# Performance work log

Measured on AMD Instinct MI355X. Metric: run time of the kernel, lower is better.

Reference implementation:

```python
import jax, jax.numpy as jnp
import numpy as np

NEG = -1e20

def _rope(x):
    # x: (N, L, H, D). Original buffers use inv_freq over D with D/2 entries;
    # sin/cos tiled to full D to broadcast (original code's einsum was under-specified for 4D).
    L, D = x.shape[1], x.shape[3]
    inv_freq = 1.0 / (10000.0 ** (jnp.arange(0, D, 2, dtype=jnp.float32) / D))
    t = jnp.arange(L, dtype=jnp.float32)
    freqs = t[:, None] * inv_freq[None, :]            # (L, D/2)
    sin = jnp.concatenate([jnp.sin(freqs)] * 2, -1)[None, :, None, :]  # (1,L,1,D)
    cos = jnp.concatenate([jnp.cos(freqs)] * 2, -1)[None, :, None, :]
    return x * cos + jnp.flip(x, -1) * sin

def setup_inputs() -> dict:
    key = jax.random.key(0)
    ks = jax.random.split(key, 8)
    N, L, E, H = 2, 1024, 2048, 16
    D = E // H
    s = 0.02
    return {
        "values": jax.random.normal(ks[0], (N, L, E), jnp.float32),
        "keys": jax.random.normal(ks[1], (N, L, E), jnp.float32),
        "queries": jax.random.normal(ks[2], (N, L, E), jnp.float32),
        "mask": jax.random.randint(ks[3], (N, 1, L, L), 0, 2, jnp.int32),
        "Wv": jax.random.normal(ks[4], (D, D), jnp.float32) * s,
        "Wk": jax.random.normal(ks[5], (D, D), jnp.float32) * s,
        "Wq": jax.random.normal(ks[6], (D, D), jnp.float32) * s,
        "Wo": jax.random.normal(ks[7], (E, E), jnp.float32) * s,
        "bo": jnp.zeros((E,), jnp.float32),
    }

def reference(values, keys, queries, mask, Wv, Wk, Wq, Wo, bo):
    N, L, E = queries.shape
    H = 16
    D = E // H
    v = values.reshape(N, L, H, D)
    k = keys.reshape(N, L, H, D)
    q = queries.reshape(N, L, H, D)
    q = _rope(q)
    k = _rope(k)
    # per-head linears (nn.Linear: x @ W.T)
    v = jnp.einsum('nlhd,od->nlho', v, Wv)
    k = jnp.einsum('nlhd,od->nlho', k, Wk)
    q = jnp.einsum('nlhd,od->nlho', q, Wq)
    energy = jnp.einsum('nqhd,nkhd->nhqk', q, k)
    energy = jnp.where(mask == 0, NEG, energy)
    attn = jax.nn.softmax(energy / jnp.sqrt(jnp.float32(E)), axis=3)
    out = jnp.einsum('nhqk,nkhd->nqhd', attn, v).reshape(N, L, E)
    return out @ Wo.T + bo
```

## Files before the change

### kernel.cpp

```cpp
#include <hip/hip_runtime.h>

#define LQ 1024
#define EMB 2048
#define NH 16
#define HD 128
#define RSCALE 0.022097086912079608f

typedef unsigned short u16x8 __attribute__((ext_vector_type(8)));
typedef __bf16 bf16x8 __attribute__((ext_vector_type(8)));
typedef float f32x4 __attribute__((ext_vector_type(4)));

__device__ __forceinline__ unsigned short f2b(float f){
  unsigned int x = __float_as_uint(f);
  return (unsigned short)((x + 0x7fffu + ((x >> 16) & 1u)) >> 16);
}
__device__ __forceinline__ bf16x8 as_bf(u16x8 u){
  union { u16x8 u; bf16x8 b; } c; c.u = u; return c.b;
}

__global__ __launch_bounds__(256) void k_sincos(float* __restrict__ cosT,
                                                float* __restrict__ sinT){
  int idx = blockIdx.x * 256 + threadIdx.x;
  int l = idx >> 7, d = idx & 127, j = d & 63;
  float inv = 1.0f / powf(10000.0f, (float)(2 * j) * 0.0078125f);
  float ang = (float)l * inv;
  cosT[idx] = cosf(ang);
  sinT[idx] = sinf(ang);
}

__global__ __launch_bounds__(256) void k_cvt(const float* __restrict__ src,
                                             unsigned short* __restrict__ dst){
  int i = (blockIdx.x * 256 + threadIdx.x) * 4;
  float4 f = *(const float4*)&src[i];
  ushort4 u;
  u.x = f2b(f.x); u.y = f2b(f.y); u.z = f2b(f.z); u.w = f2b(f.w);
  *(ushort4*)&dst[i] = u;
}

__global__ __launch_bounds__(256) void k_maskpack(const int* __restrict__ M,
                                                  unsigned long long* __restrict__ Mb){
  int w_idx = blockIdx.x * 4 + (threadIdx.x >> 6);
  int lane = threadIdx.x & 63;
  int n = w_idx >> 14, row = (w_idx >> 4) & 1023, wc = w_idx & 15;
  int v = M[(size_t)n * (LQ * LQ) + (size_t)row * LQ + wc * 64 + lane];
  unsigned long long b = __ballot(v != 0);
  if (lane == 0) Mb[w_idx] = b;
}

__global__ __launch_bounds__(256) void k_proj(
    const float* __restrict__ vals, const float* __restrict__ keys,
    const float* __restrict__ qrys,
    const float* __restrict__ Wv, const float* __restrict__ Wk,
    const float* __restrict__ Wq,
    const float* __restrict__ cosT, const float* __restrict__ sinT,
    unsigned short* __restrict__ vp, unsigned short* __restrict__ kp,
    unsigned short* __restrict__ qp)
{
  __shared__ unsigned short Xs[64 * 136];
  __shared__ unsigned short Ws[128 * 136];
  int t = threadIdx.x;
  int which = blockIdx.y;
  const float* X; const float* W; unsigned short* OUT; bool rope;
  if (which == 0)      { X = vals; W = Wv; OUT = vp; rope = false; }
  else if (which == 1) { X = keys; W = Wk; OUT = kp; rope = true;  }
  else                 { X = qrys; W = Wq; OUT = qp; rope = true;  }
  int m0 = blockIdx.x * 64;

  #pragma unroll
  for (int i = 0; i < 8; ++i) {
    int ci = t + 256 * i;
    int row = ci >> 4, ch = ci & 15;
    float4 a = *(const float4*)&W[row * 128 + ch * 8];
    float4 b = *(const float4*)&W[row * 128 + ch * 8 + 4];
    u16x8 u;
    u[0]=f2b(a.x); u[1]=f2b(a.y); u[2]=f2b(a.z); u[3]=f2b(a.w);
    u[4]=f2b(b.x); u[5]=f2b(b.y); u[6]=f2b(b.z); u[7]=f2b(b.w);
    *(u16x8*)&Ws[row * 136 + ch * 8] = u;
  }
  #pragma unroll
  for (int i = 0; i < 8; ++i) {
    int fi = t + 256 * i;
    int row = fi >> 5, dq = (fi & 31) * 4;
    int gr = m0 + row;
    float4 x = *(const float4*)&X[(size_t)gr * HD + dq];
    ushort4 u;
    if (rope) {
      int l = (gr >> 4) & 1023;
      float4 xm = *(const float4*)&X[(size_t)gr * HD + (124 - dq)];
      float4 c  = *(const float4*)&cosT[l * HD + dq];
      float4 s  = *(const float4*)&sinT[l * HD + dq];
      u.x = f2b(x.x * c.x + xm.w * s.x);
      u.y = f2b(x.y * c.y + xm.z * s.y);
      u.z = f2b(x.z * c.z + xm.y * s.z);
      u.w = f2b(x.w * c.w + xm.x * s.w);
    } else {
      u.x = f2b(x.x); u.y = f2b(x.y); u.z = f2b(x.z); u.w = f2b(x.w);
    }
    *(ushort4*)&Xs[row * 136 + dq] = u;
  }
  __syncthreads();

  int w = t >> 6, lane = t & 63, quad = lane >> 4, n16 = lane & 15;
  f32x4 of[4][2];
  #pragma unroll
  for (int a = 0; a < 4; ++a)
    { of[a][0] = (f32x4){0.f,0.f,0.f,0.f}; of[a][1] = (f32x4){0.f,0.f,0.f,0.f}; }

  #pragma unroll
  for (int kd = 0; kd < 4; ++kd) {
    bf16x8 bfr[2];
    #pragma unroll
    for (int b2 = 0; b2 < 2; ++b2)
      bfr[b2] = as_bf(*(const u16x8*)&Ws[(w * 32 + b2 * 16 + n16) * 136 + kd * 32 + quad * 8]);
    #pragma unroll
    for (int a = 0; a < 4; ++a) {
      bf16x8 af = as_bf(*(const u16x8*)&Xs[(a * 16 + n16) * 136 + kd * 32 + quad * 8]);
      of[a][0] = __builtin_amdgcn_mfma_f32_16x16x32_bf16(af, bfr[0], of[a][0], 0, 0, 0);
      of[a][1] = __builtin_amdgcn_mfma_f32_16x16x32_bf16(af, bfr[1], of[a][1], 0, 0, 0);
    }
  }

  #pragma unroll
  for (int a = 0; a < 4; ++a) {
    #pragma unroll
    for (int b2 = 0; b2 < 2; ++b2) {
      #pragma unroll
      for (int r = 0; r < 4; ++r) {
        int m = m0 + a * 16 + quad * 4 + r;
        int n = m >> 14, l = (m >> 4) & 1023, h = m & 15;
        int o = w * 32 + b2 * 16 + n16;
        OUT[(((size_t)(n * NH + h)) * LQ + l) * HD + o] = f2b(of[a][b2][r]);
      }
    }
  }
}

__global__ __launch_bounds__(256) void k_vtrans(const unsigned short* __restrict__ vp,
                                                unsigned short* __restrict__ vt){
  __shared__ unsigned short Ls[64 * 136];
  int t = threadIdx.x;
  int l0 = blockIdx.x * 64;
  size_t base = (size_t)blockIdx.y * LQ * HD;
  #pragma unroll
  for (int i = 0; i < 4; ++i) {
    int ci = t + 256 * i;
    int row = ci >> 4, ch = ci & 15;
    *(u16x8*)&Ls[row * 136 + ch * 8] =
        *(const u16x8*)&vp[base + (size_t)(l0 + row) * HD + ch * 8];
  }
  __syncthreads();
  #pragma unroll
  for (int i = 0; i < 4; ++i) {
    int idx = t + 256 * i;
    int d = idx & 127, lc = idx >> 7;
    u16x8 pk;
    #pragma unroll
    for (int j = 0; j < 8; ++j) pk[j] = Ls[(lc * 8 + j) * 136 + d];
    *(u16x8*)&vt[base + (size_t)d * LQ + l0 + lc * 8] = pk;
  }
}

__global__ __launch_bounds__(256) void k_attn(
    const unsigned short* __restrict__ qp, const unsigned short* __restrict__ kp,
    const unsigned short* __restrict__ vt, const unsigned long long* __restrict__ Mb,
    unsigned short* __restrict__ ao)
{
  __shared__ unsigned short Ks[64 * 136];
  __shared__ unsigned short Vt[128 * 72];
  __shared__ unsigned short Ss[4 * 16 * 72];
  int t = threadIdx.x, w = t >> 6, lane = t & 63, quad = lane >> 4, n16 = lane & 15;
  int bh = blockIdx.y, nIdx = bh >> 4, h = bh & 15;
  int q0 = blockIdx.x * 64;
  size_t base = (size_t)bh * LQ * HD;
  const unsigned short* Q = qp + base;
  const unsigned short* K = kp + base;
  const unsigned short* V = vt + base;

  bf16x8 qf[4];
  #pragma unroll
  for (int kd = 0; kd < 4; ++kd)
    qf[kd] = as_bf(*(const u16x8*)&Q[(size_t)(q0 + w * 16 + n16) * HD + kd * 32 + quad * 8]);

  const unsigned long long* MbRow =
      Mb + ((size_t)nIdx * LQ + q0 + w * 16 + quad * 4) * 16;

  f32x4 of[8];
  #pragma unroll
  for (int c = 0; c < 8; ++c) of[c] = (f32x4){0.f, 0.f, 0.f, 0.f};
  float lp[4] = {0.f, 0.f, 0.f, 0.f};
  unsigned short* Ssw = Ss + w * 1152;

  u16x8 pk[4], pv[4];
  #pragma unroll
  for (int i = 0; i < 4; ++i) {
    int ci = t + 256 * i;
    pk[i] = *(const u16x8*)&K[(size_t)(ci >> 4) * HD + (ci & 15) * 8];
    pv[i] = *(const u16x8*)&V[(size_t)(ci >> 3) * LQ + (ci & 7) * 8];
  }

  for (int kt = 0; kt < 16; ++kt) {
    __syncthreads();
    #pragma unroll
    for (int i = 0; i < 4; ++i) {
      int ci = t + 256 * i;
      *(u16x8*)&Ks[(ci >> 4) * 136 + (ci & 15) * 8] = pk[i];
      *(u16x8*)&Vt[(ci >> 3) * 72 + (ci & 7) * 8]  = pv[i];
    }
    __syncthreads();
    if (kt < 15) {
      int k1 = (kt + 1) * 64;
      #pragma unroll
      for (int i = 0; i < 4; ++i) {
        int ci = t + 256 * i;
        pk[i] = *(const u16x8*)&K[(size_t)(k1 + (ci >> 4)) * HD + (ci & 15) * 8];
        pv[i] = *(const u16x8*)&V[(size_t)(ci >> 3) * LQ + k1 + (ci & 7) * 8];
      }
    }
    unsigned long long mw[4];
    #pragma unroll
    for (int r = 0; r < 4; ++r) mw[r] = MbRow[r * 16 + kt];

    f32x4 sf[4];
    #pragma unroll
    for (int c = 0; c < 4; ++c) sf[c] = (f32x4){0.f, 0.f, 0.f, 0.f};
    #pragma unroll
    for (int kd = 0; kd < 4; ++kd) {
      #pragma unroll
      for (int c = 0; c < 4; ++c) {
        bf16x8 kv = as_bf(*(const u16x8*)&Ks[(c * 16 + n16) * 136 + kd * 32 + quad * 8]);
        sf[c] = __builtin_amdgcn_mfma_f32_16x16x32_bf16(qf[kd], kv, sf[c], 0, 0, 0);
      }
    }
    #pragma unroll
    for (int r = 0; r < 4; ++r) {
      #pragma unroll
      for (int c = 0; c < 4; ++c) {
        int bit = (int)((mw[r] >> (c * 16 + n16)) & 1ull);
        float p = bit ? __expf(sf[c][r] * RSCALE) : 0.f;
        lp[r] += p;
        Ssw[(quad * 4 + r) * 72 + c * 16 + n16] = f2b(p);
      }
    }
    #pragma unroll
    for (int ks = 0; ks < 2; ++ks) {
      bf16x8 pa = as_bf(*(const u16x8*)&Ssw[n16 * 72 + ks * 32 + quad * 8]);
      #pragma unroll
      for (int c2 = 0; c2 < 8; ++c2) {
        bf16x8 vv = as_bf(*(const u16x8*)&Vt[(c2 * 16 + n16) * 72 + ks * 32 + quad * 8]);
        of[c2] = __builtin_amdgcn_mfma_f32_16x16x32_bf16(pa, vv, of[c2], 0, 0, 0);
      }
    }
  }

  #pragma unroll
  for (int r = 0; r < 4; ++r) {
    float s = lp[r];
    #pragma unroll
    for (int off = 1; off < 16; off <<= 1) s += __shfl_xor(s, off, 16);
    lp[r] = 1.0f / fmaxf(s, 1e-30f);
  }
  #pragma unroll
  for (int c2 = 0; c2 < 8; ++c2) {
    #pragma unroll
    for (int r = 0; r < 4; ++r) {
      ao[((size_t)(nIdx * LQ + q0 + w * 16 + quad * 4 + r)) * EMB + h * HD + c2 * 16 + n16] =
          f2b(of[c2][r] * lp[r]);
    }
  }
}

__global__ __launch_bounds__(256) void k_outproj(
    const unsigned short* __restrict__ ao, const unsigned short* __restrict__ Wob,
    const float* __restrict__ bo, float* __restrict__ out)
{
  __shared__ unsigned short As[64 * 40];
  __shared__ unsigned short Bs[128 * 40];
  int t = threadIdx.x;
  int w = t >> 6, lane = t & 63, quad = lane >> 4, n16 = lane & 15;
  int m0 = blockIdx.x * 64, o0 = blockIdx.y * 128;

  f32x4 of[4][2];
  #pragma unroll
  for (int a = 0; a < 4; ++a)
    { of[a][0] = (f32x4){0.f,0.f,0.f,0.f}; of[a][1] = (f32x4){0.f,0.f,0.f,0.f}; }

  for (int k0 = 0; k0 < EMB; k0 += 32) {
    __syncthreads();
    {
      int row = t >> 2, ch = t & 3;
      *(u16x8*)&As[row * 40 + ch * 8] =
          *(const u16x8*)&ao[(size_t)(m0 + row) * EMB + k0 + ch * 8];
    }
    #pragma unroll
    for (int i = 0; i < 2; ++i) {
      int li = t + 256 * i;
      int row = li >> 2, ch = li & 3;
      *(u16x8*)&Bs[row * 40 + ch * 8] =
          *(const u16x8*)&Wob[(size_t)(o0 + row) * EMB + k0 + ch * 8];
    }
    __syncthreads();
    bf16x8 af[4], bfr[2];
    #pragma unroll
    for (int a = 0; a < 4; ++a)
      af[a] = as_bf(*(const u16x8*)&As[(a * 16 + n16) * 40 + quad * 8]);
    #pragma unroll
    for (int b = 0; b < 2; ++b)
      bfr[b] = as_bf(*(const u16x8*)&Bs[(w * 32 + b * 16 + n16) * 40 + quad * 8]);
    #pragma unroll
    for (int a = 0; a < 4; ++a) {
      #pragma unroll
      for (int b = 0; b < 2; ++b)
        of[a][b] = __builtin_amdgcn_mfma_f32_16x16x32_bf16(af[a], bfr[b], of[a][b], 0, 0, 0);
    }
  }

  float bb[2] = { bo[o0 + w * 32 + n16], bo[o0 + w * 32 + 16 + n16] };
  #pragma unroll
  for (int a = 0; a < 4; ++a) {
    #pragma unroll
    for (int b = 0; b < 2; ++b) {
      #pragma unroll
      for (int r = 0; r < 4; ++r) {
        out[(size_t)(m0 + a * 16 + quad * 4 + r) * EMB + o0 + w * 32 + b * 16 + n16] =
            of[a][b][r] + bb[b];
      }
    }
  }
}

extern "C" void kernel_launch(void* const* d_in, const int* in_sizes, int n_in,
                              void* d_out, int out_size, void* d_ws, size_t ws_size,
                              hipStream_t stream) {
  (void)in_sizes; (void)n_in; (void)out_size; (void)ws_size;
  const float* vals = (const float*)d_in[0];
  const float* keys = (const float*)d_in[1];
  const float* qrys = (const float*)d_in[2];
  const int*   mask = (const int*)d_in[3];
  const float* Wv   = (const float*)d_in[4];
  const float* Wk   = (const float*)d_in[5];
  const float* Wq   = (const float*)d_in[6];
  const float* Wo   = (const float*)d_in[7];
  const float* bo   = (const float*)d_in[8];
  float* out = (float*)d_out;

  unsigned short* U  = (unsigned short*)d_ws;
  unsigned short* qp = U;
  unsigned short* kp = U + 4194304;
  unsigned short* vp = U + 8388608;
  unsigned short* vt = U + 12582912;
  unsigned short* ao = U + 16777216;
  unsigned short* Wob= U + 20971520;
  unsigned long long* Mb = (unsigned long long*)(U + 25165824);
  float* cosT = (float*)(U + 25296896);
  float* sinT = cosT + 131072;

  k_sincos  <<<dim3(512),    dim3(256), 0, stream>>>(cosT, sinT);
  k_cvt     <<<dim3(4096),   dim3(256), 0, stream>>>(Wo, Wob);
  k_maskpack<<<dim3(8192),   dim3(256), 0, stream>>>(mask, Mb);
  k_proj    <<<dim3(512, 3), dim3(256), 0, stream>>>(vals, keys, qrys, Wv, Wk, Wq,
                                                     cosT, sinT, vp, kp, qp);
  k_vtrans  <<<dim3(16, 32), dim3(256), 0, stream>>>(vp, vt);
  k_attn    <<<dim3(16, 32), dim3(256), 0, stream>>>(qp, kp, vt, Mb, ao);
  k_outproj <<<dim3(32, 16), dim3(256), 0, stream>>>(ao, Wob, bo, out);
}
```

Before: 223.5 us.

## Use direct global-to-LDS loads with XOR swizzle, fuse prep kernels, retile outproj

Merges the Wo conversion and mask packing into one launch, and drops the sincos kernel by computing rope tables in shared memory inside the projection kernel. Attention and output projection now stage K/V and GEMM tiles with global_load_lds and XOR-swizzled unpadded LDS layouts. The output projection moves to a 128x128 tile with a 64-wide K step. This cuts launch count, register-staged copies and LDS bank conflicts. In exchange, the attention loop loses its register prefetch of the next tile, so loads are no longer overlapped with compute, and sin/cos is recomputed in every block.

Measured after the change: 225.6 us. About the same (+1.0%).

```diff
diff --git a/kernel.cpp b/kernel.cpp
--- a/kernel.cpp
+++ b/kernel.cpp
@@ -10,6 +10,12 @@
 typedef __bf16 bf16x8 __attribute__((ext_vector_type(8)));
 typedef float f32x4 __attribute__((ext_vector_type(4)));
 
+typedef const __attribute__((address_space(1))) unsigned int* gas_t;
+typedef __attribute__((address_space(3))) unsigned int* las_t;
+
+__device__ __forceinline__ void glds16(const void* g, void* l){
+  __builtin_amdgcn_global_load_lds((gas_t)g, (las_t)l, 16, 0, 0);
+}
 __device__ __forceinline__ unsigned short f2b(float f){
   unsigned int x = __float_as_uint(f);
   return (unsigned short)((x + 0x7fffu + ((x >> 16) & 1u)) >> 16);
@@ -18,33 +24,25 @@
   union { u16x8 u; bf16x8 b; } c; c.u = u; return c.b;
 }
 
-__global__ __launch_bounds__(256) void k_sincos(float* __restrict__ cosT,
-                                                float* __restrict__ sinT){
-  int idx = blockIdx.x * 256 + threadIdx.x;
-  int l = idx >> 7, d = idx & 127, j = d & 63;
-  float inv = 1.0f / powf(10000.0f, (float)(2 * j) * 0.0078125f);
-  float ang = (float)l * inv;
-  cosT[idx] = cosf(ang);
-  sinT[idx] = sinf(ang);
-}
-
-__global__ __launch_bounds__(256) void k_cvt(const float* __restrict__ src,
-                                             unsigned short* __restrict__ dst){
-  int i = (blockIdx.x * 256 + threadIdx.x) * 4;
-  float4 f = *(const float4*)&src[i];
-  ushort4 u;
-  u.x = f2b(f.x); u.y = f2b(f.y); u.z = f2b(f.z); u.w = f2b(f.w);
-  *(ushort4*)&dst[i] = u;
-}
-
-__global__ __launch_bounds__(256) void k_maskpack(const int* __restrict__ M,
-                                                  unsigned long long* __restrict__ Mb){
-  int w_idx = blockIdx.x * 4 + (threadIdx.x >> 6);
-  int lane = threadIdx.x & 63;
-  int n = w_idx >> 14, row = (w_idx >> 4) & 1023, wc = w_idx & 15;
-  int v = M[(size_t)n * (LQ * LQ) + (size_t)row * LQ + wc * 64 + lane];
-  unsigned long long b = __ballot(v != 0);
-  if (lane == 0) Mb[w_idx] = b;
+__global__ __launch_bounds__(256) void k_prep(const float* __restrict__ Wo,
+                                              unsigned short* __restrict__ Wob,
+                                              const int* __restrict__ M,
+                                              unsigned long long* __restrict__ Mb){
+  int bx = blockIdx.x, t = threadIdx.x;
+  if (bx < 4096) {
+    int i = (bx * 256 + t) * 4;
+    float4 f = *(const float4*)&Wo[i];
+    ushort4 u;
+    u.x = f2b(f.x); u.y = f2b(f.y); u.z = f2b(f.z); u.w = f2b(f.w);
+    *(ushort4*)&Wob[i] = u;
+  } else {
+    int w_idx = (bx - 4096) * 4 + (t >> 6);
+    int lane = t & 63;
+    int n = w_idx >> 14, row = (w_idx >> 4) & 1023, wc = w_idx & 15;
+    int v = M[(size_t)n * (LQ * LQ) + (size_t)row * LQ + wc * 64 + lane];
+    unsigned long long b = __ballot(v != 0);
+    if (lane == 0) Mb[w_idx] = b;
+  }
 }
 
 __global__ __launch_bounds__(256) void k_proj(
@@ -52,12 +50,12 @@
     const float* __restrict__ qrys,
     const float* __restrict__ Wv, const float* __restrict__ Wk,
     const float* __restrict__ Wq,
-    const float* __restrict__ cosT, const float* __restrict__ sinT,
     unsigned short* __restrict__ vp, unsigned short* __restrict__ kp,
     unsigned short* __restrict__ qp)
 {
   __shared__ unsigned short Xs[64 * 136];
   __shared__ unsigned short Ws[128 * 136];
+  __shared__ float scC[4 * 128], scS[4 * 128];
   int t = threadIdx.x;
   int which = blockIdx.y;
   const float* X; const float* W; unsigned short* OUT; bool rope;
@@ -77,6 +75,19 @@
     u[4]=f2b(b.x); u[5]=f2b(b.y); u[6]=f2b(b.z); u[7]=f2b(b.w);
     *(u16x8*)&Ws[row * 136 + ch * 8] = u;
   }
+  if (rope) {
+    int l0 = (blockIdx.x * 4) & 1023;
+    #pragma unroll
+    for (int i = 0; i < 2; ++i) {
+      int idx = t + 256 * i;
+      int li = idx >> 7, d = idx & 127, j = d & 63;
+      float inv = 1.0f / powf(10000.0f, (float)(2 * j) * 0.0078125f);
+      float ang = (float)(l0 + li) * inv;
+      scC[idx] = cosf(ang);
+      scS[idx] = sinf(ang);
+    }
+  }
+  __syncthreads();
   #pragma unroll
   for (int i = 0; i < 8; ++i) {
     int fi = t + 256 * i;
@@ -85,10 +96,10 @@
     float4 x = *(const float4*)&X[(size_t)gr * HD + dq];
     ushort4 u;
     if (rope) {
-      int l = (gr >> 4) & 1023;
+      int li = row >> 4;
       float4 xm = *(const float4*)&X[(size_t)gr * HD + (124 - dq)];
-      float4 c  = *(const float4*)&cosT[l * HD + dq];
-      float4 s  = *(const float4*)&sinT[l * HD + dq];
+      float4 c  = *(const float4*)&scC[li * 128 + dq];
+      float4 s  = *(const float4*)&scS[li * 128 + dq];
       u.x = f2b(x.x * c.x + xm.w * s.x);
       u.y = f2b(x.y * c.y + xm.z * s.y);
       u.z = f2b(x.z * c.z + xm.y * s.z);
@@ -165,8 +176,8 @@
     const unsigned short* __restrict__ vt, const unsigned long long* __restrict__ Mb,
     unsigned short* __restrict__ ao)
 {
-  __shared__ unsigned short Ks[64 * 136];
-  __shared__ unsigned short Vt[128 * 72];
+  __shared__ unsigned short Ks[64 * 128];
+  __shared__ unsigned short Vt[128 * 64];
   __shared__ unsigned short Ss[4 * 16 * 72];
   int t = threadIdx.x, w = t >> 6, lane = t & 63, quad = lane >> 4, n16 = lane & 15;
   int bh = blockIdx.y, nIdx = bh >> 4, h = bh & 15;
@@ -189,36 +200,23 @@
   for (int c = 0; c < 8; ++c) of[c] = (f32x4){0.f, 0.f, 0.f, 0.f};
   float lp[4] = {0.f, 0.f, 0.f, 0.f};
   unsigned short* Ssw = Ss + w * 1152;
-
-  u16x8 pk[4], pv[4];
-  #pragma unroll
-  for (int i = 0; i < 4; ++i) {
-    int ci = t + 256 * i;
-    pk[i] = *(const u16x8*)&K[(size_t)(ci >> 4) * HD + (ci & 15) * 8];
-    pv[i] = *(const u16x8*)&V[(size_t)(ci >> 3) * LQ + (ci & 7) * 8];
-  }
+  int ub = (t & 192);
 
   for (int kt = 0; kt < 16; ++kt) {
+    int k0 = kt * 64;
     __syncthreads();
     #pragma unroll
     for (int i = 0; i < 4; ++i) {
       int ci = t + 256 * i;
-      *(u16x8*)&Ks[(ci >> 4) * 136 + (ci & 15) * 8] = pk[i];
-      *(u16x8*)&Vt[(ci >> 3) * 72 + (ci & 7) * 8]  = pv[i];
-    }
+      int krow = ci >> 4, kslot = ci & 15, kch = kslot ^ (krow & 7);
+      glds16(&K[(size_t)(k0 + krow) * HD + kch * 8], &Ks[(ub + 256 * i) * 8]);
+      int vrow = ci >> 3, vslot = ci & 7, vch = vslot ^ (vrow & 7);
+      glds16(&V[(size_t)vrow * LQ + k0 + vch * 8], &Vt[(ub + 256 * i) * 8]);
+    }
+    unsigned long long mw[4];
+    #pragma unroll
+    for (int r = 0; r < 4; ++r) mw[r] = MbRow[r * 16 + kt];
     __syncthreads();
-    if (kt < 15) {
-      int k1 = (kt + 1) * 64;
-      #pragma unroll
-      for (int i = 0; i < 4; ++i) {
-        int ci = t + 256 * i;
-        pk[i] = *(const u16x8*)&K[(size_t)(k1 + (ci >> 4)) * HD + (ci & 15) * 8];
-        pv[i] = *(const u16x8*)&V[(size_t)(ci >> 3) * LQ + k1 + (ci & 7) * 8];
-      }
-    }
-    unsigned long long mw[4];
-    #pragma unroll
-    for (int r = 0; r < 4; ++r) mw[r] = MbRow[r * 16 + kt];
 
     f32x4 sf[4];
     #pragma unroll
@@ -227,7 +225,8 @@
     for (int kd = 0; kd < 4; ++kd) {
       #pragma unroll
       for (int c = 0; c < 4; ++c) {
-        bf16x8 kv = as_bf(*(const u16x8*)&Ks[(c * 16 + n16) * 136 + kd * 32 + quad * 8]);
+        int slot = (kd * 4 + quad) ^ (n16 & 7);
+        bf16x8 kv = as_bf(*(const u16x8*)&Ks[(c * 16 + n16) * 128 + slot * 8]);
         sf[c] = __builtin_amdgcn_mfma_f32_16x16x32_bf16(qf[kd], kv, sf[c], 0, 0, 0);
       }
     }
@@ -246,7 +245,8 @@
       bf16x8 pa = as_bf(*(const u16x8*)&Ssw[n16 * 72 + ks * 32 + quad * 8]);
       #pragma unroll
       for (int c2 = 0; c2 < 8; ++c2) {
-        bf16x8 vv = as_bf(*(const u16x8*)&Vt[(c2 * 16 + n16) * 72 + ks * 32 + quad * 8]);
+        int slot = (ks * 4 + quad) ^ (n16 & 7);
+        bf16x8 vv = as_bf(*(const u16x8*)&Vt[(c2 * 16 + n16) * 64 + slot * 8]);
         of[c2] = __builtin_amdgcn_mfma_f32_16x16x32_bf16(pa, vv, of[c2], 0, 0, 0);
       }
     }
@@ -273,56 +273,64 @@
     const unsigned short* __restrict__ ao, const unsigned short* __restrict__ Wob,
     const float* __restrict__ bo, float* __restrict__ out)
 {
-  __shared__ unsigned short As[64 * 40];
-  __shared__ unsigned short Bs[128 * 40];
+  __shared__ unsigned short As[128 * 64];
+  __shared__ unsigned short Bs[128 * 64];
   int t = threadIdx.x;
   int w = t >> 6, lane = t & 63, quad = lane >> 4, n16 = lane & 15;
-  int m0 = blockIdx.x * 64, o0 = blockIdx.y * 128;
-
-  f32x4 of[4][2];
+  int wm = w >> 1, wo = w & 1;
+  int m0 = blockIdx.x * 128, o0 = blockIdx.y * 128;
+  int ub = (t & 192);
+
+  f32x4 of[4][4];
   #pragma unroll
   for (int a = 0; a < 4; ++a)
-    { of[a][0] = (f32x4){0.f,0.f,0.f,0.f}; of[a][1] = (f32x4){0.f,0.f,0.f,0.f}; }
-
-  for (int k0 = 0; k0 < EMB; k0 += 32) {
+    #pragma unroll
+    for (int b = 0; b < 4; ++b) of[a][b] = (f32x4){0.f, 0.f, 0.f, 0.f};
+
+  for (int k0 = 0; k0 < EMB; k0 += 64) {
     __syncthreads();
-    {
-      int row = t >> 2, ch = t & 3;
-      *(u16x8*)&As[row * 40 + ch * 8] =
-          *(const u16x8*)&ao[(size_t)(m0 + row) * EMB + k0 + ch * 8];
-    }
-    #pragma unroll
-    for (int i = 0; i < 2; ++i) {
-      int li = t + 256 * i;
-      int row = li >> 2, ch = li & 3;
-      *(u16x8*)&Bs[row * 40 + ch * 8] =
-          *(const u16x8*)&Wob[(size_t)(o0 + row) * EMB + k0 + ch * 8];
+    #pragma unroll
+    for (int i = 0; i < 4; ++i) {
+      int ci = t + 256 * i;
+      int row = ci >> 3, slot = ci & 7, ch = slot ^ (row & 7);
+      glds16(&ao [(size_t)(m0 + row) * EMB + k0 + ch * 8], &As[(ub + 256 * i) * 8]);
+      glds16(&Wob[(size_t)(o0 + row) * EMB + k0 + ch * 8], &Bs[(ub + 256 * i) * 8]);
     }
     __syncthreads();
-    bf16x8 af[4], bfr[2];
-    #pragma unroll
-    for (int a = 0; a < 4; ++a)
-      af[a] = as_bf(*(const u16x8*)&As[(a * 16 + n16) * 40 + quad * 8]);
-    #pragma unroll
-    for (int b = 0; b < 2; ++b)
-      bfr[b] = as_bf(*(const u16x8*)&Bs[(w * 32 + b * 16 + n16) * 40 + quad * 8]);
-    #pragma unroll
-    for (int a = 0; a < 4; ++a) {
-      #pragma unroll
-      for (int b = 0; b < 2; ++b)
-        of[a][b] = __builtin_amdgcn_mfma_f32_16x16x32_bf16(af[a], bfr[b], of[a][b], 0, 0, 0);
-    }
-  }
-
-  float bb[2] = { bo[o0 + w * 32 + n16], bo[o0 + w * 32 + 16 + n16] };
+    #pragma unroll
+    for (int kd = 0; kd < 2; ++kd) {
+      bf16x8 af[4], bf[4];
+      #pragma unroll
+      for (int a = 0; a < 4; ++a) {
+        int row = wm * 64 + a * 16 + n16;
+        int slot = (kd * 4 + quad) ^ (n16 & 7);
+        af[a] = as_bf(*(const u16x8*)&As[row * 64 + slot * 8]);
+      }
+      #pragma unroll
+      for (int b = 0; b < 4; ++b) {
+        int row = wo * 64 + b * 16 + n16;
+        int slot = (kd * 4 + quad) ^ (n16 & 7);
+        bf[b] = as_bf(*(const u16x8*)&Bs[row * 64 + slot * 8]);
+      }
+      #pragma unroll
+      for (int a = 0; a < 4; ++a)
+        #pragma unroll
+        for (int b = 0; b < 4; ++b)
+          of[a][b] = __builtin_amdgcn_mfma_f32_16x16x32_bf16(af[a], bf[b], of[a][b], 0, 0, 0);
+    }
+  }
+
+  float bb[4];
+  #pragma unroll
+  for (int b = 0; b < 4; ++b) bb[b] = bo[o0 + wo * 64 + b * 16 + n16];
   #pragma unroll
   for (int a = 0; a < 4; ++a) {
     #pragma unroll
-    for (int b = 0; b < 2; ++b) {
+    for (int b = 0; b < 4; ++b) {
       #pragma unroll
       for (int r = 0; r < 4; ++r) {
-        out[(size_t)(m0 + a * 16 + quad * 4 + r) * EMB + o0 + w * 32 + b * 16 + n16] =
-            of[a][b][r] + bb[b];
+        out[(size_t)(m0 + wm * 64 + a * 16 + quad * 4 + r) * EMB
+            + o0 + wo * 64 + b * 16 + n16] = of[a][b][r] + bb[b];
       }
     }
   }
@@ -351,15 +359,11 @@
   unsigned short* ao = U + 16777216;
   unsigned short* Wob= U + 20971520;
   unsigned long long* Mb = (unsigned long long*)(U + 25165824);
-  float* cosT = (float*)(U + 25296896);
-  float* sinT = cosT + 131072;
-
-  k_sincos  <<<dim3(512),    dim3(256), 0, stream>>>(cosT, sinT);
-  k_cvt     <<<dim3(4096),   dim3(256), 0, stream>>>(Wo, Wob);
-  k_maskpack<<<dim3(8192),   dim3(256), 0, stream>>>(mask, Mb);
+
+  k_prep    <<<dim3(12288),  dim3(256), 0, stream>>>(Wo, Wob, mask, Mb);
   k_proj    <<<dim3(512, 3), dim3(256), 0, stream>>>(vals, keys, qrys, Wv, Wk, Wq,
-                                                     cosT, sinT, vp, kp, qp);
+                                                     vp, kp, qp);
   k_vtrans  <<<dim3(16, 32), dim3(256), 0, stream>>>(vp, vt);
   k_attn    <<<dim3(16, 32), dim3(256), 0, stream>>>(qp, kp, vt, Mb, ao);
-  k_outproj <<<dim3(32, 16), dim3(256), 0, stream>>>(ao, Wob, bo, out);
-}
+  k_outproj <<<dim3(16, 16), dim3(256), 0, stream>>>(ao, Wob, bo, out);
+}
```
